# Optimization experiments

Hardware: AMD Instinct MI355X
Metric: run time of the kernel (lower is better)

Reference implementation:

```python
import jax, jax.numpy as jnp
import numpy as np

B, S, D = 4096, 200, 64
EPS = 1e-3  # keras BatchNormalization default epsilon

def setup_inputs() -> dict:
    key = jax.random.key(0)
    ks = jax.random.split(key, 8)
    return {
        "em": jax.random.normal(ks[0], (B, D), jnp.float32),
        "eu": jax.random.normal(ks[1], (B, D), jnp.float32),
        "Xu": jax.random.normal(ks[2], (B, S, D), jnp.float32),
        "W1": jax.random.normal(ks[3], (4 * D, 64), jnp.float32) * 0.05,
        "b1": jnp.zeros((64,), jnp.float32),
        "W2": jax.random.normal(ks[4], (64, 32), jnp.float32) * 0.1,
        "b2": jnp.zeros((32,), jnp.float32),
        "W3": jax.random.normal(ks[5], (32, 1), jnp.float32) * 0.1,
        "b3": jnp.zeros((1,), jnp.float32),
        "gamma": jnp.ones((2 * D,), jnp.float32),
        "beta": jnp.zeros((2 * D,), jnp.float32),
        "mov_mean": jnp.zeros((2 * D,), jnp.float32),
        "mov_var": jnp.ones((2 * D,), jnp.float32),
    }

def reference(em, eu, Xu, W1, b1, W2, b2, W3, b3, gamma, beta, mov_mean, mov_var):
    # DIN attention: query = em tiled over seq, key = value = Xu
    q = jnp.broadcast_to(em[:, None, :], Xu.shape)            # [B,S,D]
    info = jnp.concatenate([q, Xu, q - Xu, q * Xu], axis=-1)  # [B,S,4D]
    h = jax.nn.relu(info @ W1 + b1)                           # [B,S,64]
    h = jax.nn.relu(h @ W2 + b2)                              # [B,S,32]
    logits = (h @ W3 + b3)[..., 0]                            # [B,S]
    w = jax.nn.softmax(logits, axis=-1)                       # [B,S]
    pooled = jnp.einsum('bs,bsd->bd', w, Xu)                  # [B,D]
    info_all = jnp.concatenate([pooled, em], axis=-1)         # [B,2D]
    bn = (info_all - mov_mean) * jax.lax.rsqrt(mov_var + EPS) * gamma + beta
    return jnp.concatenate([bn, eu], axis=-1)                 # [B,2D+Du]
```

## Files before the change

### kernel.cpp

```cpp
#include <hip/hip_runtime.h>
#include <hip/hip_bf16.h>
#include <math.h>

typedef __bf16 bf16_t;
typedef bf16_t bf16x2 __attribute__((ext_vector_type(2)));
typedef bf16_t bf16x8 __attribute__((ext_vector_type(8)));
typedef float  f32x4  __attribute__((ext_vector_type(4)));
typedef int    i32x4  __attribute__((ext_vector_type(4)));
typedef unsigned int u32;

#define SEQ 200
#define DD  64

#define MFMA(a, b, c) __builtin_amdgcn_mfma_f32_16x16x32_bf16((a), (b), (c), 0, 0, 0)

__global__ __launch_bounds__(256) void prep_kernel(
    const float* __restrict__ W1, const float* __restrict__ W2,
    bf16_t* __restrict__ Wbc, bf16_t* __restrict__ W1dt,
    bf16_t* __restrict__ W2t, float* __restrict__ W1sT)
{
  const int tid = threadIdx.x;
  for (int i = tid; i < 64 * 64; i += 256) {
    int rp = i >> 6, k = i & 63;
    int j = rp >> 4, mm = rp & 15;
    int n = ((j & 1) << 2) | ((j >> 1) << 5) | ((mm >> 2) << 3) | (mm & 3);
    Wbc[i]  = (bf16_t)(W1[(64 + k) * 64 + n] - W1[(128 + k) * 64 + n]);
    W1dt[i] = (bf16_t)(W1[(192 + k) * 64 + n]);
    W1sT[i] = W1[k * 64 + rp] + W1[(128 + k) * 64 + rp];
  }
  for (int i = tid; i < 32 * 64; i += 256) {
    int n = i >> 6, k = i & 63;
    W2t[i] = (bf16_t)(W2[k * 32 + n]);
  }
}

__device__ __forceinline__ u32 pk2(float x, float y) {
  bf16x2 t;
  t[0] = (bf16_t)fmaxf(x, 0.f);
  t[1] = (bf16_t)fmaxf(y, 0.f);
  return __builtin_bit_cast(u32, t);
}

#define XR4(v) { v += __shfl_xor(v, 1); v += __shfl_xor(v, 2); \
                 v += __shfl_xor(v, 4); v += __shfl_xor(v, 8); }
#define XM4(v) { v = fmaxf(v, __shfl_xor(v, 1)); v = fmaxf(v, __shfl_xor(v, 2)); \
                 v = fmaxf(v, __shfl_xor(v, 4)); v = fmaxf(v, __shfl_xor(v, 8)); }

#define LOADT(t, Y0, Y1, Y2, Y3) do {                                          \
    int row_ = 16 * (t) + l16;                                                 \
    row_ = row_ < SEQ ? row_ : (SEQ - 1);                                      \
    const float4* p_ = Xr + (row_ * 16 + 2 * g);                               \
    Y0 = p_[0]; Y1 = p_[1]; Y2 = p_[8]; Y3 = p_[9];                            \
  } while (0)

#define PROC(MASKED, Y0, Y1, Y2, Y3) do {                                      \
    bf16x8 a0_, a1_;                                                           \
    a0_[0]=(bf16_t)Y0.x; a0_[1]=(bf16_t)Y0.y; a0_[2]=(bf16_t)Y0.z; a0_[3]=(bf16_t)Y0.w; \
    a0_[4]=(bf16_t)Y1.x; a0_[5]=(bf16_t)Y1.y; a0_[6]=(bf16_t)Y1.z; a0_[7]=(bf16_t)Y1.w; \
    a1_[0]=(bf16_t)Y2.x; a1_[1]=(bf16_t)Y2.y; a1_[2]=(bf16_t)Y2.z; a1_[3]=(bf16_t)Y2.w; \
    a1_[4]=(bf16_t)Y3.x; a1_[5]=(bf16_t)Y3.y; a1_[6]=(bf16_t)Y3.z; a1_[7]=(bf16_t)Y3.w; \
    f32x4 zz_ = {0.f, 0.f, 0.f, 0.f};                                          \
    f32x4 c0_ = MFMA(bB00, a0_, zz_); c0_ = MFMA(bB01, a1_, c0_);              \
    f32x4 c1_ = MFMA(bB10, a0_, zz_); c1_ = MFMA(bB11, a1_, c1_);              \
    f32x4 c2_ = MFMA(bB20, a0_, zz_); c2_ = MFMA(bB21, a1_, c2_);              \
    f32x4 c3_ = MFMA(bB30, a0_, zz_); c3_ = MFMA(bB31, a1_, c3_);              \
    i32x4 f0_ = { (int)pk2(c0_[0] + Q00, c0_[1] + Q01),                        \
                  (int)pk2(c0_[2] + Q02, c0_[3] + Q03),                        \
                  (int)pk2(c1_[0] + Q10, c1_[1] + Q11),                        \
                  (int)pk2(c1_[2] + Q12, c1_[3] + Q13) };                      \
    i32x4 f1_ = { (int)pk2(c2_[0] + Q20, c2_[1] + Q21),                        \
                  (int)pk2(c2_[2] + Q22, c2_[3] + Q23),                        \
                  (int)pk2(c3_[0] + Q30, c3_[1] + Q31),                        \
                  (int)pk2(c3_[2] + Q32, c3_[3] + Q33) };                      \
    bf16x8 hf0_ = __builtin_bit_cast(bf16x8, f0_);                             \
    bf16x8 hf1_ = __builtin_bit_cast(bf16x8, f1_);                             \
    f32x4 d0_ = MFMA(W2fA0, hf0_, zz_); d0_ = MFMA(W2fA1, hf1_, d0_);          \
    f32x4 d1_ = MFMA(W2fB0, hf0_, zz_); d1_ = MFMA(W2fB1, hf1_, d1_);          \
    float pr_ = fmaxf(d0_[0] + b2lo.x, 0.f) * w3lo.x                           \
              + fmaxf(d0_[1] + b2lo.y, 0.f) * w3lo.y                           \
              + fmaxf(d0_[2] + b2lo.z, 0.f) * w3lo.z                           \
              + fmaxf(d0_[3] + b2lo.w, 0.f) * w3lo.w                           \
              + fmaxf(d1_[0] + b2hi.x, 0.f) * w3hi.x                           \
              + fmaxf(d1_[1] + b2hi.y, 0.f) * w3hi.y                           \
              + fmaxf(d1_[2] + b2hi.z, 0.f) * w3hi.z                           \
              + fmaxf(d1_[3] + b2hi.w, 0.f) * w3hi.w;                          \
    pr_ += __shfl_xor(pr_, 16);                                                \
    pr_ += __shfl_xor(pr_, 32);                                                \
    float lv_ = pr_ + b3s;                                                     \
    if (MASKED && l16 >= 8) lv_ = -INFINITY;                                   \
    if (!__all(lv_ <= m + 8.f)) {        \
      float tm_ = lv_;                                                         \
      XM4(tm_)                                                                 \
      float mn_ = fmaxf(m, tm_);                                               \
      float al_ = __expf(m - mn_);                                             \
      Zp *= al_;                                                               \
      Pa0 *= al_; Pa1 *= al_; Pa2 *= al_; Pa3 *= al_;                          \
      Pa4 *= al_; Pa5 *= al_; Pa6 *= al_; Pa7 *= al_;                          \
      Pb0 *= al_; Pb1 *= al_; Pb2 *= al_; Pb3 *= al_;                          \
      Pb4 *= al_; Pb5 *= al_; Pb6 *= al_; Pb7 *= al_;                          \
      m = mn_;                                                                 \
    }                                                                          \
    float ee_ = __expf(lv_ - m);                                               \
    Zp += ee_;                                                                 \
    Pa0 += ee_ * (float)a0_[0]; Pa1 += ee_ * (float)a0_[1];                    \
    Pa2 += ee_ * (float)a0_[2]; Pa3 += ee_ * (float)a0_[3];                    \
    Pa4 += ee_ * (float)a0_[4]; Pa5 += ee_ * (float)a0_[5];                    \
    Pa6 += ee_ * (float)a0_[6]; Pa7 += ee_ * (float)a0_[7];                    \
    Pb0 += ee_ * (float)a1_[0]; Pb1 += ee_ * (float)a1_[1];                    \
    Pb2 += ee_ * (float)a1_[2]; Pb3 += ee_ * (float)a1_[3];                    \
    Pb4 += ee_ * (float)a1_[4]; Pb5 += ee_ * (float)a1_[5];                    \
    Pb6 += ee_ * (float)a1_[6]; Pb7 += ee_ * (float)a1_[7];                    \
  } while (0)

__global__ __launch_bounds__(256, 3) void din_kernel(
    const float* __restrict__ em, const float* __restrict__ eu,
    const float* __restrict__ Xu, const float* __restrict__ b1,
    const float* __restrict__ b2, const float* __restrict__ W3,
    const float* __restrict__ b3, const float* __restrict__ gam,
    const float* __restrict__ bet, const float* __restrict__ mmean,
    const float* __restrict__ mvar, const bf16_t* __restrict__ Wbc,
    const bf16_t* __restrict__ W1dt, const bf16_t* __restrict__ W2t,
    const float* __restrict__ W1sT, float* __restrict__ out, int Btot)
{
  const int tid  = threadIdx.x;
  const int lane = tid & 63;
  const int wid  = tid >> 6;
  const int g    = lane >> 4;
  const int l16  = lane & 15;
  const int b    = blockIdx.x * 4 + wid;
  if (b >= Btot) return;

  const float* emr  = em + (size_t)b * DD;
  const float  em_l = emr[lane];
  float4 ef0 = *(const float4*)&emr[8 * g];
  float4 ef1 = *(const float4*)&emr[8 * g + 4];
  float4 ef2 = *(const float4*)&emr[32 + 8 * g];
  float4 ef3 = *(const float4*)&emr[32 + 8 * g + 4];

  const bf16x8* Wbc8  = (const bf16x8*)Wbc;
  const bf16x8* W1dt8 = (const bf16x8*)W1dt;
  const bf16x8* W2t8  = (const bf16x8*)W2t;
#define MKBB(NAME, J, C, E0, E1)                                               \
  bf16x8 NAME; {                                                               \
    bf16x8 w_ = Wbc8[(16 * (J) + l16) * 8 + 4 * (C) + g];                      \
    bf16x8 d_ = W1dt8[(16 * (J) + l16) * 8 + 4 * (C) + g];                     \
    NAME[0] = (bf16_t)((float)w_[0] + E0.x * (float)d_[0]);                    \
    NAME[1] = (bf16_t)((float)w_[1] + E0.y * (float)d_[1]);                    \
    NAME[2] = (bf16_t)((float)w_[2] + E0.z * (float)d_[2]);                    \
    NAME[3] = (bf16_t)((float)w_[3] + E0.w * (float)d_[3]);                    \
    NAME[4] = (bf16_t)((float)w_[4] + E1.x * (float)d_[4]);                    \
    NAME[5] = (bf16_t)((float)w_[5] + E1.y * (float)d_[5]);                    \
    NAME[6] = (bf16_t)((float)w_[6] + E1.z * (float)d_[6]);                    \
    NAME[7] = (bf16_t)((float)w_[7] + E1.w * (float)d_[7]);                    \
  }
  MKBB(bB00, 0, 0, ef0, ef1) MKBB(bB01, 0, 1, ef2, ef3)
  MKBB(bB10, 1, 0, ef0, ef1) MKBB(bB11, 1, 1, ef2, ef3)
  MKBB(bB20, 2, 0, ef0, ef1) MKBB(bB21, 2, 1, ef2, ef3)
  MKBB(bB30, 3, 0, ef0, ef1) MKBB(bB31, 3, 1, ef2, ef3)
#undef MKBB

  const bf16x8 W2fA0 = W2t8[l16 * 8 + g];
  const bf16x8 W2fA1 = W2t8[l16 * 8 + 4 + g];
  const bf16x8 W2fB0 = W2t8[(16 + l16) * 8 + g];
  const bf16x8 W2fB1 = W2t8[(16 + l16) * 8 + 4 + g];

  const float4 b2lo = *(const float4*)&b2[4 * g];
  const float4 b2hi = *(const float4*)&b2[16 + 4 * g];
  const float4 w3lo = *(const float4*)&W3[4 * g];
  const float4 w3hi = *(const float4*)&W3[16 + 4 * g];
  const float  b3s  = b3[0];

  float q = b1[lane];
  {
    const float4* wq = (const float4*)(W1sT + lane * 64);
    #pragma unroll
    for (int dd = 0; dd < 16; ++dd) {
      float4 wv = wq[dd];
      float ex = __shfl(em_l, 4 * dd + 0);
      float ey = __shfl(em_l, 4 * dd + 1);
      float ez = __shfl(em_l, 4 * dd + 2);
      float ew = __shfl(em_l, 4 * dd + 3);
      q += ex * wv.x + ey * wv.y + ez * wv.z + ew * wv.w;
    }
  }
#define MKQ(NAME, J, R) const float NAME = __shfl(q, (((J)&1)<<2) + (((J)>>1)<<5) + 8*g + (R));
  MKQ(Q00, 0, 0) MKQ(Q01, 0, 1) MKQ(Q02, 0, 2) MKQ(Q03, 0, 3)
  MKQ(Q10, 1, 0) MKQ(Q11, 1, 1) MKQ(Q12, 1, 2) MKQ(Q13, 1, 3)
  MKQ(Q20, 2, 0) MKQ(Q21, 2, 1) MKQ(Q22, 2, 2) MKQ(Q23, 2, 3)
  MKQ(Q30, 3, 0) MKQ(Q31, 3, 1) MKQ(Q32, 3, 2) MKQ(Q33, 3, 3)
#undef MKQ

  float m = -INFINITY, Zp = 0.f;
  float Pa0 = 0.f, Pa1 = 0.f, Pa2 = 0.f, Pa3 = 0.f;
  float Pa4 = 0.f, Pa5 = 0.f, Pa6 = 0.f, Pa7 = 0.f;
  float Pb0 = 0.f, Pb1 = 0.f, Pb2 = 0.f, Pb3 = 0.f;
  float Pb4 = 0.f, Pb5 = 0.f, Pb6 = 0.f, Pb7 = 0.f;

  const float4* Xr = (const float4*)(Xu + (size_t)b * SEQ * DD);

  float4 A0, A1, A2, A3, B0, B1, B2, B3;
  LOADT(0, A0, A1, A2, A3);
  #pragma unroll 1
  for (int t = 0; t < 12; t += 2) {
    LOADT(t + 1, B0, B1, B2, B3);
    PROC(0, A0, A1, A2, A3);
    LOADT(t + 2, A0, A1, A2, A3);
    PROC(0, B0, B1, B2, B3);
  }
  PROC(1, A0, A1, A2, A3);

  float Z = Zp;
  XR4(Z)
  const float invZ = 1.f / Z;
  XR4(Pa0) XR4(Pa1) XR4(Pa2) XR4(Pa3) XR4(Pa4) XR4(Pa5) XR4(Pa6) XR4(Pa7)
  XR4(Pb0) XR4(Pb1) XR4(Pb2) XR4(Pb3) XR4(Pb4) XR4(Pb5) XR4(Pb6) XR4(Pb7)

  const int  gsrc = (lane >> 3) & 3;
  const int  srcl = 16 * gsrc + l16;
  const int  esel = lane & 7;
  const bool hi   = lane >= 32;
  float pooled = 0.f, t_;
  t_ = __shfl(Pa0, srcl); if (!hi && esel == 0) pooled = t_;
  t_ = __shfl(Pa1, srcl); if (!hi && esel == 1) pooled = t_;
  t_ = __shfl(Pa2, srcl); if (!hi && esel == 2) pooled = t_;
  t_ = __shfl(Pa3, srcl); if (!hi && esel == 3) pooled = t_;
  t_ = __shfl(Pa4, srcl); if (!hi && esel == 4) pooled = t_;
  t_ = __shfl(Pa5, srcl); if (!hi && esel == 5) pooled = t_;
  t_ = __shfl(Pa6, srcl); if (!hi && esel == 6) pooled = t_;
  t_ = __shfl(Pa7, srcl); if (!hi && esel == 7) pooled = t_;
  t_ = __shfl(Pb0, srcl); if (hi && esel == 0) pooled = t_;
  t_ = __shfl(Pb1, srcl); if (hi && esel == 1) pooled = t_;
  t_ = __shfl(Pb2, srcl); if (hi && esel == 2) pooled = t_;
  t_ = __shfl(Pb3, srcl); if (hi && esel == 3) pooled = t_;
  t_ = __shfl(Pb4, srcl); if (hi && esel == 4) pooled = t_;
  t_ = __shfl(Pb5, srcl); if (hi && esel == 5) pooled = t_;
  t_ = __shfl(Pb6, srcl); if (hi && esel == 6) pooled = t_;
  t_ = __shfl(Pb7, srcl); if (hi && esel == 7) pooled = t_;
  pooled *= invZ;

  float o0 = (pooled - mmean[lane]) * rsqrtf(mvar[lane] + 1e-3f) * gam[lane] + bet[lane];
  float o1 = (em_l - mmean[64 + lane]) * rsqrtf(mvar[64 + lane] + 1e-3f) * gam[64 + lane] + bet[64 + lane];
  float o2 = eu[(size_t)b * 64 + lane];
  float* ob = out + (size_t)b * 192;
  ob[lane]       = o0;
  ob[64 + lane]  = o1;
  ob[128 + lane] = o2;
}

extern "C" void kernel_launch(void* const* d_in, const int* in_sizes, int n_in,
                              void* d_out, int out_size, void* d_ws, size_t ws_size,
                              hipStream_t stream) {
  const float* em = (const float*)d_in[0];
  const float* eu = (const float*)d_in[1];
  const float* Xu = (const float*)d_in[2];
  const float* W1 = (const float*)d_in[3];
  const float* b1 = (const float*)d_in[4];
  const float* W2 = (const float*)d_in[5];
  const float* b2 = (const float*)d_in[6];
  const float* W3 = (const float*)d_in[7];
  const float* b3 = (const float*)d_in[8];
  const float* ga = (const float*)d_in[9];
  const float* be = (const float*)d_in[10];
  const float* mm = (const float*)d_in[11];
  const float* mv = (const float*)d_in[12];
  int B = in_sizes[0] / DD;

  float*  W1sT = (float*)d_ws;
  bf16_t* Wbc  = (bf16_t*)((char*)d_ws + 64 * 64 * 4);
  bf16_t* W1dt = Wbc + 64 * 64;
  bf16_t* W2t  = W1dt + 64 * 64;

  prep_kernel<<<1, 256, 0, stream>>>(W1, W2, Wbc, W1dt, W2t, W1sT);
  din_kernel<<<(B + 3) / 4, 256, 0, stream>>>(em, eu, Xu, b1, b2, W3, b3, ga, be,
                                              mm, mv, Wbc, W1dt, W2t, W1sT,
                                              (float*)d_out, B);
}
```

Baseline: 333.6 us.

## Split each batch row's sequence across four waves and merge softmax partials in LDS

Each block now handles one batch row: the four waves take interleaved 16-row tiles of the sequence, keep their own online-softmax max, sum and pooled partials, then combine them through shared memory with rescaling, and wave 0 writes the output. This gives each wave less serial work and more parallelism per row, but every wave still rebuilds the per-row weight fragments and query bias, so the setup cost is now paid four times per row. The query bias is also folded into the MFMA accumulator init, and em is read directly as float4 instead of being broadcast with shuffles.

```diff
diff --git a/kernel.cpp b/kernel.cpp
--- a/kernel.cpp
+++ b/kernel.cpp
@@ -59,19 +59,19 @@
     a0_[4]=(bf16_t)Y1.x; a0_[5]=(bf16_t)Y1.y; a0_[6]=(bf16_t)Y1.z; a0_[7]=(bf16_t)Y1.w; \
     a1_[0]=(bf16_t)Y2.x; a1_[1]=(bf16_t)Y2.y; a1_[2]=(bf16_t)Y2.z; a1_[3]=(bf16_t)Y2.w; \
     a1_[4]=(bf16_t)Y3.x; a1_[5]=(bf16_t)Y3.y; a1_[6]=(bf16_t)Y3.z; a1_[7]=(bf16_t)Y3.w; \
+    f32x4 q0_ = {Q00, Q01, Q02, Q03};                                          \
+    f32x4 q1_ = {Q10, Q11, Q12, Q13};                                          \
+    f32x4 q2_ = {Q20, Q21, Q22, Q23};                                          \
+    f32x4 q3_ = {Q30, Q31, Q32, Q33};                                          \
     f32x4 zz_ = {0.f, 0.f, 0.f, 0.f};                                          \
-    f32x4 c0_ = MFMA(bB00, a0_, zz_); c0_ = MFMA(bB01, a1_, c0_);              \
-    f32x4 c1_ = MFMA(bB10, a0_, zz_); c1_ = MFMA(bB11, a1_, c1_);              \
-    f32x4 c2_ = MFMA(bB20, a0_, zz_); c2_ = MFMA(bB21, a1_, c2_);              \
-    f32x4 c3_ = MFMA(bB30, a0_, zz_); c3_ = MFMA(bB31, a1_, c3_);              \
-    i32x4 f0_ = { (int)pk2(c0_[0] + Q00, c0_[1] + Q01),                        \
-                  (int)pk2(c0_[2] + Q02, c0_[3] + Q03),                        \
-                  (int)pk2(c1_[0] + Q10, c1_[1] + Q11),                        \
-                  (int)pk2(c1_[2] + Q12, c1_[3] + Q13) };                      \
-    i32x4 f1_ = { (int)pk2(c2_[0] + Q20, c2_[1] + Q21),                        \
-                  (int)pk2(c2_[2] + Q22, c2_[3] + Q23),                        \
-                  (int)pk2(c3_[0] + Q30, c3_[1] + Q31),                        \
-                  (int)pk2(c3_[2] + Q32, c3_[3] + Q33) };                      \
+    f32x4 c0_ = MFMA(bB00, a0_, q0_); c0_ = MFMA(bB01, a1_, c0_);              \
+    f32x4 c1_ = MFMA(bB10, a0_, q1_); c1_ = MFMA(bB11, a1_, c1_);              \
+    f32x4 c2_ = MFMA(bB20, a0_, q2_); c2_ = MFMA(bB21, a1_, c2_);              \
+    f32x4 c3_ = MFMA(bB30, a0_, q3_); c3_ = MFMA(bB31, a1_, c3_);              \
+    i32x4 f0_ = { (int)pk2(c0_[0], c0_[1]), (int)pk2(c0_[2], c0_[3]),          \
+                  (int)pk2(c1_[0], c1_[1]), (int)pk2(c1_[2], c1_[3]) };        \
+    i32x4 f1_ = { (int)pk2(c2_[0], c2_[1]), (int)pk2(c2_[2], c2_[3]),          \
+                  (int)pk2(c3_[0], c3_[1]), (int)pk2(c3_[2], c3_[3]) };        \
     bf16x8 hf0_ = __builtin_bit_cast(bf16x8, f0_);                             \
     bf16x8 hf1_ = __builtin_bit_cast(bf16x8, f1_);                             \
     f32x4 d0_ = MFMA(W2fA0, hf0_, zz_); d0_ = MFMA(W2fA1, hf1_, d0_);          \
@@ -120,15 +120,17 @@
     const float* __restrict__ bet, const float* __restrict__ mmean,
     const float* __restrict__ mvar, const bf16_t* __restrict__ Wbc,
     const bf16_t* __restrict__ W1dt, const bf16_t* __restrict__ W2t,
-    const float* __restrict__ W1sT, float* __restrict__ out, int Btot)
+    const float* __restrict__ W1sT, float* __restrict__ out)
 {
+  __shared__ float Pl[4][64];
+  __shared__ float mZs[4][2];
+
   const int tid  = threadIdx.x;
   const int lane = tid & 63;
   const int wid  = tid >> 6;
   const int g    = lane >> 4;
   const int l16  = lane & 15;
-  const int b    = blockIdx.x * 4 + wid;
-  if (b >= Btot) return;
+  const int b    = blockIdx.x;
 
   const float* emr  = em + (size_t)b * DD;
   const float  em_l = emr[lane];
@@ -173,14 +175,12 @@
   float q = b1[lane];
   {
     const float4* wq = (const float4*)(W1sT + lane * 64);
+    const float4* eq = (const float4*)emr;
     #pragma unroll
     for (int dd = 0; dd < 16; ++dd) {
       float4 wv = wq[dd];
-      float ex = __shfl(em_l, 4 * dd + 0);
-      float ey = __shfl(em_l, 4 * dd + 1);
-      float ez = __shfl(em_l, 4 * dd + 2);
-      float ew = __shfl(em_l, 4 * dd + 3);
-      q += ex * wv.x + ey * wv.y + ez * wv.z + ew * wv.w;
+      float4 ev = eq[dd];
+      q += ev.x * wv.x + ev.y * wv.y + ev.z * wv.z + ev.w * wv.w;
     }
   }
 #define MKQ(NAME, J, R) const float NAME = __shfl(q, (((J)&1)<<2) + (((J)>>1)<<5) + 8*g + (R));
@@ -199,19 +199,21 @@
   const float4* Xr = (const float4*)(Xu + (size_t)b * SEQ * DD);
 
   float4 A0, A1, A2, A3, B0, B1, B2, B3;
-  LOADT(0, A0, A1, A2, A3);
-  #pragma unroll 1
-  for (int t = 0; t < 12; t += 2) {
-    LOADT(t + 1, B0, B1, B2, B3);
+  LOADT(wid, A0, A1, A2, A3);
+  LOADT(wid + 4, B0, B1, B2, B3);
+  PROC(0, A0, A1, A2, A3);
+  LOADT(wid + 8, A0, A1, A2, A3);
+  PROC(0, B0, B1, B2, B3);
+  if (wid == 0) {
+    LOADT(12, B0, B1, B2, B3);
     PROC(0, A0, A1, A2, A3);
-    LOADT(t + 2, A0, A1, A2, A3);
-    PROC(0, B0, B1, B2, B3);
-  }
-  PROC(1, A0, A1, A2, A3);
-
-  float Z = Zp;
-  XR4(Z)
-  const float invZ = 1.f / Z;
+    PROC(1, B0, B1, B2, B3);
+  } else {
+    PROC(0, A0, A1, A2, A3);
+  }
+
+  float Zw = Zp;
+  XR4(Zw)
   XR4(Pa0) XR4(Pa1) XR4(Pa2) XR4(Pa3) XR4(Pa4) XR4(Pa5) XR4(Pa6) XR4(Pa7)
   XR4(Pb0) XR4(Pb1) XR4(Pb2) XR4(Pb3) XR4(Pb4) XR4(Pb5) XR4(Pb6) XR4(Pb7)
 
@@ -219,32 +221,46 @@
   const int  srcl = 16 * gsrc + l16;
   const int  esel = lane & 7;
   const bool hi   = lane >= 32;
-  float pooled = 0.f, t_;
-  t_ = __shfl(Pa0, srcl); if (!hi && esel == 0) pooled = t_;
-  t_ = __shfl(Pa1, srcl); if (!hi && esel == 1) pooled = t_;
-  t_ = __shfl(Pa2, srcl); if (!hi && esel == 2) pooled = t_;
-  t_ = __shfl(Pa3, srcl); if (!hi && esel == 3) pooled = t_;
-  t_ = __shfl(Pa4, srcl); if (!hi && esel == 4) pooled = t_;
-  t_ = __shfl(Pa5, srcl); if (!hi && esel == 5) pooled = t_;
-  t_ = __shfl(Pa6, srcl); if (!hi && esel == 6) pooled = t_;
-  t_ = __shfl(Pa7, srcl); if (!hi && esel == 7) pooled = t_;
-  t_ = __shfl(Pb0, srcl); if (hi && esel == 0) pooled = t_;
-  t_ = __shfl(Pb1, srcl); if (hi && esel == 1) pooled = t_;
-  t_ = __shfl(Pb2, srcl); if (hi && esel == 2) pooled = t_;
-  t_ = __shfl(Pb3, srcl); if (hi && esel == 3) pooled = t_;
-  t_ = __shfl(Pb4, srcl); if (hi && esel == 4) pooled = t_;
-  t_ = __shfl(Pb5, srcl); if (hi && esel == 5) pooled = t_;
-  t_ = __shfl(Pb6, srcl); if (hi && esel == 6) pooled = t_;
-  t_ = __shfl(Pb7, srcl); if (hi && esel == 7) pooled = t_;
-  pooled *= invZ;
-
-  float o0 = (pooled - mmean[lane]) * rsqrtf(mvar[lane] + 1e-3f) * gam[lane] + bet[lane];
-  float o1 = (em_l - mmean[64 + lane]) * rsqrtf(mvar[64 + lane] + 1e-3f) * gam[64 + lane] + bet[64 + lane];
-  float o2 = eu[(size_t)b * 64 + lane];
-  float* ob = out + (size_t)b * 192;
-  ob[lane]       = o0;
-  ob[64 + lane]  = o1;
-  ob[128 + lane] = o2;
+  float pw = 0.f, t_;
+  t_ = __shfl(Pa0, srcl); if (!hi && esel == 0) pw = t_;
+  t_ = __shfl(Pa1, srcl); if (!hi && esel == 1) pw = t_;
+  t_ = __shfl(Pa2, srcl); if (!hi && esel == 2) pw = t_;
+  t_ = __shfl(Pa3, srcl); if (!hi && esel == 3) pw = t_;
+  t_ = __shfl(Pa4, srcl); if (!hi && esel == 4) pw = t_;
+  t_ = __shfl(Pa5, srcl); if (!hi && esel == 5) pw = t_;
+  t_ = __shfl(Pa6, srcl); if (!hi && esel == 6) pw = t_;
+  t_ = __shfl(Pa7, srcl); if (!hi && esel == 7) pw = t_;
+  t_ = __shfl(Pb0, srcl); if (hi && esel == 0) pw = t_;
+  t_ = __shfl(Pb1, srcl); if (hi && esel == 1) pw = t_;
+  t_ = __shfl(Pb2, srcl); if (hi && esel == 2) pw = t_;
+  t_ = __shfl(Pb3, srcl); if (hi && esel == 3) pw = t_;
+  t_ = __shfl(Pb4, srcl); if (hi && esel == 4) pw = t_;
+  t_ = __shfl(Pb5, srcl); if (hi && esel == 5) pw = t_;
+  t_ = __shfl(Pb6, srcl); if (hi && esel == 6) pw = t_;
+  t_ = __shfl(Pb7, srcl); if (hi && esel == 7) pw = t_;
+
+  Pl[wid][lane] = pw;
+  if (lane == 0) { mZs[wid][0] = m; mZs[wid][1] = Zw; }
+  __syncthreads();
+
+  if (wid == 0) {
+    float m0 = mZs[0][0], m1 = mZs[1][0], m2 = mZs[2][0], m3 = mZs[3][0];
+    float ms = fmaxf(fmaxf(m0, m1), fmaxf(m2, m3));
+    float s0 = __expf(m0 - ms), s1 = __expf(m1 - ms);
+    float s2 = __expf(m2 - ms), s3 = __expf(m3 - ms);
+    float Zt = s0 * mZs[0][1] + s1 * mZs[1][1] + s2 * mZs[2][1] + s3 * mZs[3][1];
+    float Pt = s0 * Pl[0][lane] + s1 * Pl[1][lane]
+             + s2 * Pl[2][lane] + s3 * Pl[3][lane];
+    float pooled = Pt / Zt;
+
+    float o0 = (pooled - mmean[lane]) * rsqrtf(mvar[lane] + 1e-3f) * gam[lane] + bet[lane];
+    float o1 = (em_l - mmean[64 + lane]) * rsqrtf(mvar[64 + lane] + 1e-3f) * gam[64 + lane] + bet[64 + lane];
+    float o2 = eu[(size_t)b * 64 + lane];
+    float* ob = out + (size_t)b * 192;
+    ob[lane]       = o0;
+    ob[64 + lane]  = o1;
+    ob[128 + lane] = o2;
+  }
 }
 
 extern "C" void kernel_launch(void* const* d_in, const int* in_sizes, int n_in,
@@ -271,7 +287,7 @@
   bf16_t* W2t  = W1dt + 64 * 64;
 
   prep_kernel<<<1, 256, 0, stream>>>(W1, W2, Wbc, W1dt, W2t, W1sT);
-  din_kernel<<<(B + 3) / 4, 256, 0, stream>>>(em, eu, Xu, b1, b2, W3, b3, ga, be,
-                                              mm, mv, Wbc, W1dt, W2t, W1sT,
-                                              (float*)d_out, B);
-}
+  din_kernel<<<B, 256, 0, stream>>>(em, eu, Xu, b1, b2, W3, b3, ga, be,
+                                    mm, mv, Wbc, W1dt, W2t, W1sT,
+                                    (float*)d_out);
+}
```

Measured after the change: 371.4 us. 11.3% more time.
